# Kernel optimization log

Measured on AMD Instinct MI355X. Metric: run time of the kernel, lower is better.

The kernel has to match this reference:

```python
import jax, jax.numpy as jnp
import numpy as np

B, S, D, H, Dh, A_N = 2, 1024, 512, 8, 64, 18
HID = H * Dh        # 512, equals in_features
FFN = 4 * D         # SwiGLU hidden (ratio=4)
EPS = 1e-6


def rmsnorm(x, scale):
    return x * jax.lax.rsqrt(jnp.mean(jnp.square(x), axis=-1, keepdims=True) + EPS) * scale


def setup_inputs() -> dict:
    key = jax.random.key(0)
    ks = jax.random.split(key, 16)
    lecun = lambda k, shp: jax.random.normal(k, shp, jnp.float32) * (1.0 / np.sqrt(shp[0]))
    return {
        "x": jax.random.normal(ks[0], (B, S, D), jnp.float32),
        "action": jax.random.randint(ks[1], (B, S), 0, A_N, jnp.int32),
        "mask": jnp.zeros((B, S), jnp.int32),
        "carry": jnp.zeros((B, H, Dh, Dh), jnp.float32),
        "norm1_scale": jnp.ones((D,), jnp.float32),
        "wq": lecun(ks[2], (D, HID)),
        "wk": lecun(ks[3], (D, HID)),
        "wv": lecun(ks[4], (D, HID)),
        "w_beta": lecun(ks[5], (D, H)),
        "embed": jax.random.normal(ks[6], (A_N, HID), jnp.float32) * 0.02,
        "w_alpha": lecun(ks[7], (HID, H)),
        "w_bu": lecun(ks[8], (HID, HID)),
        "w_bv": lecun(ks[9], (HID, HID)),
        "norm_attn_scale": jnp.ones((HID,), jnp.float32),
        "w_out": lecun(ks[10], (HID, D)),
        "b_out": jnp.zeros((D,), jnp.float32),
        "norm2_scale": jnp.ones((D,), jnp.float32),
        "w_gate": lecun(ks[11], (D, FFN)),
        "w_val": lecun(ks[12], (D, FFN)),
        "w_ffn": lecun(ks[13], (FFN, D)),
    }


def reference(x, action, mask, carry, norm1_scale, wq, wk, wv, w_beta, embed,
              w_alpha, w_bu, w_bv, norm_attn_scale, w_out, b_out,
              norm2_scale, w_gate, w_val, w_ffn):
    dt = x.dtype
    h = rmsnorm(x, norm1_scale)
    # projections -> [B,S,H,Dh]
    q = jax.nn.silu(h @ wq).reshape(B, S, H, Dh)
    k = jax.nn.silu(h @ wk).reshape(B, S, H, Dh)
    v = (h @ wv).reshape(B, S, H, Dh)
    beta = jax.nn.sigmoid(h @ w_beta)                       # [B,S,H]
    ae = embed[action]                                      # [B,S,HID]
    alpha = jax.nn.sigmoid(ae @ w_alpha)                    # [B,S,H]
    b_u = (ae @ w_bu).reshape(B, S, H, Dh)
    b_v = (ae @ w_bv).reshape(B, S, H, Dh)
    q = q / (jnp.linalg.norm(q, axis=-1, keepdims=True) + EPS)
    k = k / (jnp.linalg.norm(k, axis=-1, keepdims=True) + EPS)
    eye = jnp.eye(Dh, dtype=dt)
    # delta = I - beta * k k^T   -> [B,S,H,Dh,Dh]
    delta = eye - beta[..., None, None] * jnp.einsum("bshi,bshj->bshij", k, k)
    m = mask.astype(dt)[:, :, None, None, None]
    decay = alpha[..., None, None] * delta * (1.0 - m)
    drift = jnp.einsum("bshi,bshj->bshij", b_u, b_v)
    write = beta[..., None, None] * jnp.einsum("bshi,bshj->bshij", v, k)
    update = drift @ delta + write

    def binop(lhs, rhs):
        a_i, b_i = lhs
        a_j, b_j = rhs
        return (a_i @ a_j, b_i @ a_j + b_j)

    cumdecay, hs = jax.lax.associative_scan(jax.vmap(binop), (decay, update), axis=1)
    hs = carry[:, None] @ cumdecay + hs                     # [B,S,H,Dh,Dh]
    attn = jnp.einsum("bshij,bshj->bshi", hs, q).reshape(B, S, HID)
    attn = rmsnorm(attn, norm_attn_scale)
    y = attn @ w_out + b_out
    skip = y + x
    h2 = rmsnorm(skip, norm2_scale)
    ffn = (jax.nn.silu(h2 @ w_gate) * (h2 @ w_val)) @ w_ffn
    return (hs[:, -1], skip + ffn)
```

## Files before the change

kernel.cpp:

```cpp
#include <hip/hip_runtime.h>
#include <hip/hip_bf16.h>
#include <cstdint>
#include <cstddef>

using bf16 = __hip_bfloat16;
typedef __attribute__((ext_vector_type(8))) short bf16x8;
typedef __attribute__((ext_vector_type(4))) float f32x4;

static constexpr int B_ = 2, S_ = 1024, D_ = 512, H_ = 8;
static constexpr int M_ = B_ * S_;
static constexpr int CHUNKS_ = 32, CLEN_ = 32;
static constexpr float EPS_ = 1e-6f;

__device__ __forceinline__ float sigmoidf_(float x) { return 1.0f / (1.0f + __expf(-x)); }

__device__ __forceinline__ short bf_hi(float v, float& rem) {
  bf16 h = __float2bfloat16(v);
  rem = v - __bfloat162float(h);
  return *(short*)&h;
}
__device__ __forceinline__ short bf_of(float v) {
  bf16 h = __float2bfloat16(v);
  return *(short*)&h;
}

struct TJob { const float* src; bf16* dst; int K, N, base, xf; };
struct TTab { TJob j[9]; };

__global__ __launch_bounds__(256) void k_transpose_all(TTab tab) {
  __shared__ float tile[32][33];
  int blk = blockIdx.x;
  int ji = 0;
#pragma unroll
  for (int t = 1; t < 9; ++t) if (tab.j[t].base <= blk) ji = t;
  const float* W = tab.j[ji].src;
  bf16* Wt = tab.j[ji].dst;
  int K = tab.j[ji].K, N = tab.j[ji].N, xf = tab.j[ji].xf;
  int rel = blk - tab.j[ji].base;
  int nb = N >> 5;
  int n0 = (rel % nb) * 32, k0 = (rel / nb) * 32;
  int tx = threadIdx.x, ty = threadIdx.y;
#pragma unroll
  for (int r = ty; r < 32; r += 8) tile[r][tx] = W[(size_t)(k0 + r) * N + n0 + tx];
  __syncthreads();
#pragma unroll
  for (int r = ty; r < 32; r += 8) {
    int n = n0 + r;
    int drow = n;
    if (xf == 1) drow = ((n >> 5) << 6) + (n & 31);
    else if (xf == 2) drow = ((n >> 5) << 6) + (n & 31) + 32;
    Wt[(size_t)drow * K + k0 + tx] = __float2bfloat16(tile[tx][r]);
  }
}

__global__ __launch_bounds__(256) void k_rmsnorm(const float* __restrict__ x,
                                                 const float* __restrict__ scale,
                                                 float* __restrict__ outf,
                                                 bf16* __restrict__ outb) {
  int m = blockIdx.x, tid = threadIdx.x;
  const float* row = x + (size_t)m * D_;
  float2 v = *(const float2*)(row + tid * 2);
  float ss = v.x * v.x + v.y * v.y;
#pragma unroll
  for (int o = 1; o < 64; o <<= 1) ss += __shfl_xor(ss, o);
  __shared__ float wsum[4];
  if ((tid & 63) == 0) wsum[tid >> 6] = ss;
  __syncthreads();
  float tot = wsum[0] + wsum[1] + wsum[2] + wsum[3];
  float rs = rsqrtf(tot * (1.0f / (float)D_) + EPS_);
  float2 sc = *(const float2*)(scale + tid * 2);
  float o0 = v.x * rs * sc.x, o1 = v.y * rs * sc.y;
  if (outf) {
    float2 o; o.x = o0; o.y = o1;
    *(float2*)(outf + (size_t)m * D_ + tid * 2) = o;
  }
  if (outb) {
    bf16* p = outb + (size_t)m * D_ + tid * 2;
    p[0] = __float2bfloat16(o0); p[1] = __float2bfloat16(o1);
  }
}

__global__ __launch_bounds__(256) void k_gather(const int* __restrict__ action,
                                                const float* __restrict__ embed,
                                                float* __restrict__ aef, bf16* __restrict__ aeb) {
  int m = blockIdx.x, tid = threadIdx.x;
  int a = action[m];
  float2 v = *(const float2*)(embed + (size_t)a * 512 + tid * 2);
  *(float2*)(aef + (size_t)m * 512 + tid * 2) = v;
  bf16* p = aeb + (size_t)m * 512 + tid * 2;
  p[0] = __float2bfloat16(v.x); p[1] = __float2bfloat16(v.y);
}

__global__ __launch_bounds__(256) void k_dot8x2(const float* __restrict__ hF,
                                                const float* __restrict__ aeF,
                                                const float* __restrict__ W1,
                                                const float* __restrict__ W2,
                                                float* __restrict__ o1,
                                                float* __restrict__ o2) {
  int m = blockIdx.x, tid = threadIdx.x;
  float x0 = hF[(size_t)m * D_ + tid], x1 = hF[(size_t)m * D_ + 256 + tid];
  float y0 = aeF[(size_t)m * D_ + tid], y1 = aeF[(size_t)m * D_ + 256 + tid];
  float p[8], q[8];
#pragma unroll
  for (int j = 0; j < 8; ++j) {
    p[j] = x0 * W1[tid * 8 + j] + x1 * W1[(tid + 256) * 8 + j];
    q[j] = y0 * W2[tid * 8 + j] + y1 * W2[(tid + 256) * 8 + j];
  }
#pragma unroll
  for (int j = 0; j < 8; ++j) {
#pragma unroll
    for (int o = 1; o < 64; o <<= 1) {
      p[j] += __shfl_xor(p[j], o);
      q[j] += __shfl_xor(q[j], o);
    }
  }
  __shared__ float sacc[4][16];
  if ((tid & 63) == 0) {
#pragma unroll
    for (int j = 0; j < 8; ++j) { sacc[tid >> 6][j] = p[j]; sacc[tid >> 6][8 + j] = q[j]; }
  }
  __syncthreads();
  if (tid < 8) {
    float s = sacc[0][tid] + sacc[1][tid] + sacc[2][tid] + sacc[3][tid];
    o1[(size_t)m * 8 + tid] = sigmoidf_(s);
  } else if (tid < 16) {
    int j = tid - 8;
    float s = sacc[0][8 + j] + sacc[1][8 + j] + sacc[2][8 + j] + sacc[3][8 + j];
    o2[(size_t)m * 8 + j] = sigmoidf_(s);
  }
}

__global__ __launch_bounds__(256) void k_qknorm_dots(float* __restrict__ qkv,
                                                     const float* __restrict__ buv,
                                                     const float* __restrict__ betaF,
                                                     const float* __restrict__ alphaF,
                                                     const int* __restrict__ mask,
                                                     float* __restrict__ scal8) {
  int blk = blockIdx.x * 4 + (threadIdx.x >> 6);
  int m = blk >> 3, h = blk & 7, t = threadIdx.x & 63;
  size_t qi = (size_t)m * 1536 + h * 64 + t;
  float q = qkv[qi], k = qkv[qi + 512];
  float bv = buv[(size_t)m * 1024 + 512 + h * 64 + t];
  float qs = q * q, ks = k * k;
#pragma unroll
  for (int o = 1; o < 64; o <<= 1) { qs += __shfl_xor(qs, o); ks += __shfl_xor(ks, o); }
  float qn = q / (sqrtf(qs) + EPS_);
  float kn = k / (sqrtf(ks) + EPS_);
  qkv[qi] = qn; qkv[qi + 512] = kn;
  float d0 = kn * qn, d1 = kn * bv, d2 = bv * qn;
#pragma unroll
  for (int o = 1; o < 64; o <<= 1) {
    d0 += __shfl_xor(d0, o); d1 += __shfl_xor(d1, o); d2 += __shfl_xor(d2, o);
  }
  if (t == 0) {
    int mh = m * 8 + h;
    float4 s4;
    s4.x = betaF[mh];
    s4.y = alphaF[mh] * (1.0f - (float)mask[m]);
    s4.z = d0; s4.w = d1;
    *(float4*)(scal8 + (size_t)mh * 8) = s4;
    scal8[(size_t)mh * 8 + 4] = d2;
  }
}

template <int EPI>
__global__ __launch_bounds__(256) void k_gemm2(const bf16* __restrict__ A,
                                               const bf16* __restrict__ Bt,
                                               void* __restrict__ Cv, int M, int N, int K,
                                               int actSplit, const float* __restrict__ bias,
                                               const float* __restrict__ res) {
  __shared__ bf16 As[2][64 * 32];
  __shared__ bf16 Bs[2][64 * 32];
  const int tid = threadIdx.x;
  const int wave = tid >> 6, lane = tid & 63;
  const int wm = wave >> 1, wn = wave & 1;
  const int m0 = blockIdx.y * 64, n0 = blockIdx.x * 64;
  const int lr = lane & 15, lg = lane >> 4;
  const int srow = (wave << 4) | (lane >> 2);
  const int skb = (lane & 3) << 3;
  const bf16* ga = A + (size_t)(m0 + srow) * K + skb;
  const bf16* gb = Bt + (size_t)(n0 + srow) * K + skb;

  f32x4 acc[2][2];
#pragma unroll
  for (int i = 0; i < 2; ++i)
#pragma unroll
    for (int j = 0; j < 2; ++j) acc[i][j] = (f32x4){0.f, 0.f, 0.f, 0.f};

  const int nk = K >> 5;
  int4 ar = *(const int4*)ga;
  int4 br = *(const int4*)gb;
  for (int t = 0; t < nk; ++t) {
    bf16* asb = &As[t & 1][0];
    bf16* bsb = &Bs[t & 1][0];
    *(int4*)(asb + tid * 8) = ar;
    *(int4*)(bsb + tid * 8) = br;
    __syncthreads();
    if (t + 1 < nk) {
      ar = *(const int4*)(ga + ((size_t)(t + 1) << 5));
      br = *(const int4*)(gb + ((size_t)(t + 1) << 5));
    }
    bf16x8 af[2], bfr[2];
#pragma unroll
    for (int mm = 0; mm < 2; ++mm)
      af[mm] = *(const bf16x8*)(asb + (wm * 32 + mm * 16 + lr) * 32 + lg * 8);
#pragma unroll
    for (int nn = 0; nn < 2; ++nn)
      bfr[nn] = *(const bf16x8*)(bsb + (wn * 32 + nn * 16 + lr) * 32 + lg * 8);
#pragma unroll
    for (int mm = 0; mm < 2; ++mm)
#pragma unroll
      for (int nn = 0; nn < 2; ++nn)
        acc[mm][nn] = __builtin_amdgcn_mfma_f32_16x16x32_bf16(af[mm], bfr[nn], acc[mm][nn], 0, 0, 0);
  }

  if constexpr (EPI == 4) {
    __syncthreads();
    float* gateL = (float*)&As[0][0];
    float* valL = (float*)&Bs[0][0];
    float* dstL = wn ? valL : gateL;
#pragma unroll
    for (int mm = 0; mm < 2; ++mm)
#pragma unroll
      for (int nn = 0; nn < 2; ++nn)
#pragma unroll
        for (int r = 0; r < 4; ++r)
          dstL[(wm * 32 + mm * 16 + lg * 4 + r) * 32 + nn * 16 + lr] = acc[mm][nn][r];
    __syncthreads();
    bf16* Cb = (bf16*)Cv;
    int row = tid >> 2, c0 = (tid & 3) * 8;
    bf16x8 o;
#pragma unroll
    for (int e = 0; e < 8; ++e) {
      float g = gateL[row * 32 + c0 + e];
      float v = valL[row * 32 + c0 + e];
      o[e] = bf_of(g * sigmoidf_(g) * v);
    }
    *(int4*)(Cb + (size_t)(m0 + row) * 2048 + blockIdx.x * 32 + c0) = *(int4*)&o;
  } else {
    float* C = (float*)Cv;
#pragma unroll
    for (int mm = 0; mm < 2; ++mm) {
#pragma unroll
      for (int nn = 0; nn < 2; ++nn) {
#pragma unroll
        for (int r = 0; r < 4; ++r) {
          int row = m0 + wm * 32 + mm * 16 + lg * 4 + r;
          int col = n0 + wn * 32 + nn * 16 + lr;
          float v = acc[mm][nn][r];
          if constexpr (EPI == 1) {
            if (col < actSplit) v = v * sigmoidf_(v);
          }
          if constexpr (EPI == 2) v += bias[col] + res[(size_t)row * N + col];
          if constexpr (EPI == 3) v += res[(size_t)row * N + col];
          C[(size_t)row * N + col] = v;
        }
      }
    }
  }
}

struct alignas(16) StepC {
  float k[16], bv[16], q[16];
  float v_i, bu_i, beta, g, kq, kbv, bvq;
};

__device__ __forceinline__ void load_stepc(StepC& sd,
    const float* __restrict__ qkv, const float* __restrict__ buv,
    const float* __restrict__ scal8, int m, int h, int i, int j0, bool withq) {
  const float* qb = qkv + (size_t)m * 1536 + h * 64;
  const float* bb = buv + (size_t)m * 1024 + h * 64;
#pragma unroll
  for (int p = 0; p < 4; ++p) *(float4*)&sd.k[p * 4] = *(const float4*)(qb + 512 + j0 + p * 4);
#pragma unroll
  for (int p = 0; p < 4; ++p) *(float4*)&sd.bv[p * 4] = *(const float4*)(bb + 512 + j0 + p * 4);
  if (withq) {
#pragma unroll
    for (int p = 0; p < 4; ++p) *(float4*)&sd.q[p * 4] = *(const float4*)(qb + j0 + p * 4);
  }
  sd.v_i = qb[1024 + i];
  sd.bu_i = bb[i];
  const float* sp = scal8 + (size_t)(m * 8 + h) * 8;
  float4 s4 = *(const float4*)sp;
  sd.beta = s4.x; sd.g = s4.y; sd.kq = s4.z; sd.kbv = s4.w;
  if (withq) sd.bvq = sp[4];
}

__device__ __forceinline__ void step_fold(float P[16], float U[16], const StepC& sd) {
  float Pk = 0.f, Uk = 0.f;
#pragma unroll
  for (int jj = 0; jj < 16; ++jj) { Pk += P[jj] * sd.k[jj]; Uk += U[jj] * sd.k[jj]; }
  Pk += __shfl_xor(Pk, 1); Pk += __shfl_xor(Pk, 2);
  Uk += __shfl_xor(Uk, 1); Uk += __shfl_xor(Uk, 2);
  float gb = sd.g * sd.beta;
  float cP = gb * Pk;
  float Ai = sd.beta * sd.v_i - gb * Uk - sd.bu_i * sd.beta * sd.kbv;
#pragma unroll
  for (int jj = 0; jj < 16; ++jj) {
    P[jj] = sd.g * P[jj] - cP * sd.k[jj];
    U[jj] = sd.g * U[jj] + Ai * sd.k[jj] + sd.bu_i * sd.bv[jj];
  }
}

__device__ __forceinline__ void step_apply(float hs[16], const StepC& sd,
                                           float* __restrict__ attn_addr, bool writer) {
  float u = 0.f, w = 0.f;
#pragma unroll
  for (int jj = 0; jj < 16; ++jj) { u += hs[jj] * sd.k[jj]; w += hs[jj] * sd.q[jj]; }
  u += __shfl_xor(u, 1); u += __shfl_xor(u, 2);
  w += __shfl_xor(w, 1); w += __shfl_xor(w, 2);
  float a_i = sd.beta * sd.v_i - sd.g * sd.beta * u;
  float c = sd.beta * sd.kbv;
#pragma unroll
  for (int jj = 0; jj < 16; ++jj) {
    float bvp = sd.bv[jj] - c * sd.k[jj];
    hs[jj] = sd.g * hs[jj] + a_i * sd.k[jj] + sd.bu_i * bvp;
  }
  if (writer) *attn_addr = sd.g * w + a_i * sd.kq + sd.bu_i * (sd.bvq - c * sd.kq);
}

__global__ __launch_bounds__(256) void k_scan_chunk(
    const float* __restrict__ qkv, const float* __restrict__ buv,
    const float* __restrict__ scal8, bf16* __restrict__ PtHi,
    bf16* __restrict__ PtLo, float* __restrict__ Ut) {
  int blk = blockIdx.x, bh = blk >> 5, c = blk & (CHUNKS_ - 1);
  int b = bh >> 3, h = bh & 7;
  int tid = threadIdx.x, i = tid >> 2, q4 = tid & 3, j0 = q4 * 16;
  alignas(16) float P[16], U[16];
#pragma unroll
  for (int jj = 0; jj < 16; ++jj) { P[jj] = (j0 + jj == i) ? 1.f : 0.f; U[jj] = 0.f; }
  int m0 = b * S_ + c * CLEN_;
  StepC A, Bs;
  load_stepc(A, qkv, buv, scal8, m0, h, i, j0, false);
  load_stepc(Bs, qkv, buv, scal8, m0 + 1, h, i, j0, false);
  for (int s = 0; s < CLEN_; s += 2) {
    step_fold(P, U, A);
    if (s + 2 < CLEN_) load_stepc(A, qkv, buv, scal8, m0 + s + 2, h, i, j0, false);
    step_fold(P, U, Bs);
    if (s + 3 < CLEN_) load_stepc(Bs, qkv, buv, scal8, m0 + s + 3, h, i, j0, false);
  }
  const size_t base = ((size_t)bh * CHUNKS_ + c) * 4096;
#pragma unroll
  for (int jj = 0; jj < 16; ++jj) {
    int j = j0 + jj;
    float pv = P[jj];
    float rem;
    short ph = bf_hi(pv, rem);
    short pl = bf_of(rem);
    ((short*)PtHi)[base + (size_t)j * 64 + i] = ph;
    ((short*)PtLo)[base + (size_t)j * 64 + i] = pl;
    Ut[base + (size_t)j * 64 + i] = U[jj];
  }
}

#define PREFETCH_(SET, CIDX)                                                     \
  {                                                                              \
    const size_t cbo_ = (size_t)(CIDX) * 4096;                                   \
    _Pragma("unroll") for (int mt = 0; mt < 4; ++mt) {                           \
      _Pragma("unroll") for (int ks = 0; ks < 2; ++ks) {                         \
        size_t off_ = cbo_ + (size_t)(16 * mt + lr) * 64 + ks * 32 + lg * 8;     \
        aH[SET][mt][ks] = *(const bf16x8*)(PH + off_);                           \
        aL[SET][mt][ks] = *(const bf16x8*)(PL + off_);                           \
      }                                                                          \
      _Pragma("unroll") for (int r = 0; r < 4; ++r)                              \
        u[SET][mt][r] = UB[cbo_ + (size_t)(16 * mt + 4 * lg + r) * 64 + col0 + lr]; \
    }                                                                            \
  }

#define CHAINSTEP_(SET, NSET, CIDX)                                              \
  {                                                                              \
    if ((CIDX) + 1 < CHUNKS_) PREFETCH_(NSET, (CIDX) + 1);                       \
    _Pragma("unroll") for (int mt = 0; mt < 4; ++mt)                             \
      _Pragma("unroll") for (int r = 0; r < 4; ++r)                              \
        HB[(size_t)(CIDX) * 4096 + (size_t)(16 * mt + 4 * lg + r) * 64 + col0 + lr] = st[mt][r]; \
    bf16x8 bH[2], bL[2];                                                         \
    _Pragma("unroll") for (int ks = 0; ks < 2; ++ks) {                           \
      _Pragma("unroll") for (int e = 0; e < 8; ++e) {                            \
        int src_ = (2 * (lg & 1) + (e >> 2)) * 16 + lr;                          \
        float va_ = __shfl(st[2 * ks][e & 3], src_);                             \
        float vb_ = __shfl(st[2 * ks + 1][e & 3], src_);                         \
        float bv_ = (lg & 2) ? vb_ : va_;                                        \
        float rem_;                                                              \
        bH[ks][e] = bf_hi(bv_, rem_);                                            \
        bL[ks][e] = bf_of(rem_);                                                 \
      }                                                                          \
    }                                                                            \
    f32x4 stn[4];                                                                \
    _Pragma("unroll") for (int mt = 0; mt < 4; ++mt) {                           \
      f32x4 a_ = u[SET][mt];                                                     \
      _Pragma("unroll") for (int ks = 0; ks < 2; ++ks) {                         \
        a_ = __builtin_amdgcn_mfma_f32_16x16x32_bf16(aH[SET][mt][ks], bH[ks], a_, 0, 0, 0); \
        a_ = __builtin_amdgcn_mfma_f32_16x16x32_bf16(aH[SET][mt][ks], bL[ks], a_, 0, 0, 0); \
        a_ = __builtin_amdgcn_mfma_f32_16x16x32_bf16(aL[SET][mt][ks], bH[ks], a_, 0, 0, 0); \
      }                                                                          \
      stn[mt] = a_;                                                              \
    }                                                                            \
    _Pragma("unroll") for (int mt = 0; mt < 4; ++mt) st[mt] = stn[mt];           \
  }

__global__ __launch_bounds__(64, 1) void k_chain3(
    const bf16* __restrict__ PtHi, const bf16* __restrict__ PtLo,
    const float* __restrict__ Ut, const float* __restrict__ carry,
    float* __restrict__ Hbuf, float* __restrict__ out_hs) {
  const int bh = blockIdx.x >> 2, cb = blockIdx.x & 3, col0 = cb * 16;
  const int lane = threadIdx.x & 63, lr = lane & 15, lg = lane >> 4;
  const short* PH = (const short*)PtHi + (size_t)bh * CHUNKS_ * 4096;
  const short* PL = (const short*)PtLo + (size_t)bh * CHUNKS_ * 4096;
  const float* UB = Ut + (size_t)bh * CHUNKS_ * 4096;
  float* HB = Hbuf + (size_t)bh * CHUNKS_ * 4096;

  f32x4 st[4];
#pragma unroll
  for (int mt = 0; mt < 4; ++mt)
    st[mt] = *(const f32x4*)(carry + ((size_t)bh * 64 + col0 + lr) * 64 + 16 * mt + 4 * lg);

  bf16x8 aH[2][4][2], aL[2][4][2];
  f32x4 u[2][4];
  PREFETCH_(0, 0);
  for (int c = 0; c < CHUNKS_; c += 2) {
    CHAINSTEP_(0, 1, c);
    CHAINSTEP_(1, 0, c + 1);
  }
#pragma unroll
  for (int mt = 0; mt < 4; ++mt)
    *(f32x4*)(out_hs + ((size_t)bh * 64 + col0 + lr) * 64 + 16 * mt + 4 * lg) = st[mt];
}

__global__ __launch_bounds__(256) void k_apply_chunk(
    const float* __restrict__ qkv, const float* __restrict__ buv,
    const float* __restrict__ scal8, const float* __restrict__ Hbuf,
    float* __restrict__ attn) {
  int blk = blockIdx.x, bh = blk >> 5, c = blk & (CHUNKS_ - 1);
  int b = bh >> 3, h = bh & 7;
  int tid = threadIdx.x, i = tid >> 2, q4 = tid & 3, j0 = q4 * 16;
  bool writer = (q4 == 0);
  alignas(16) float hs[16];
  const float* hb = Hbuf + ((size_t)bh * CHUNKS_ + c) * 4096;
#pragma unroll
  for (int jj = 0; jj < 16; ++jj) hs[jj] = hb[(size_t)(j0 + jj) * 64 + i];
  int m0 = b * S_ + c * CLEN_;
  StepC A, Bs;
  load_stepc(A, qkv, buv, scal8, m0, h, i, j0, true);
  load_stepc(Bs, qkv, buv, scal8, m0 + 1, h, i, j0, true);
  for (int s = 0; s < CLEN_; s += 2) {
    step_apply(hs, A, attn + ((size_t)(m0 + s) * 512 + h * 64 + i), writer);
    if (s + 2 < CLEN_) load_stepc(A, qkv, buv, scal8, m0 + s + 2, h, i, j0, true);
    step_apply(hs, Bs, attn + ((size_t)(m0 + s + 1) * 512 + h * 64 + i), writer);
    if (s + 3 < CLEN_) load_stepc(Bs, qkv, buv, scal8, m0 + s + 3, h, i, j0, true);
  }
}

extern "C" void kernel_launch(void* const* d_in, const int* in_sizes, int n_in,
                              void* d_out, int out_size, void* d_ws, size_t ws_size,
                              hipStream_t stream) {
  const float* x      = (const float*)d_in[0];
  const int*   action = (const int*)d_in[1];
  const int*   mask   = (const int*)d_in[2];
  const float* carry  = (const float*)d_in[3];
  const float* n1s    = (const float*)d_in[4];
  const float* wq     = (const float*)d_in[5];
  const float* wk     = (const float*)d_in[6];
  const float* wv     = (const float*)d_in[7];
  const float* wbeta  = (const float*)d_in[8];
  const float* embed  = (const float*)d_in[9];
  const float* walpha = (const float*)d_in[10];
  const float* wbu    = (const float*)d_in[11];
  const float* wbv    = (const float*)d_in[12];
  const float* nas    = (const float*)d_in[13];
  const float* wout   = (const float*)d_in[14];
  const float* bout   = (const float*)d_in[15];
  const float* n2s    = (const float*)d_in[16];
  const float* wgate  = (const float*)d_in[17];
  const float* wval   = (const float*)d_in[18];
  const float* wffn   = (const float*)d_in[19];

  float* out_hs  = (float*)d_out;
  float* out_ffn = (float*)d_out + 65536;

  char* p = (char*)d_ws;
  auto alloc = [&](size_t bytes) -> char* {
    char* r = p; p += (bytes + 255) & ~(size_t)255; return r;
  };
  bf16*  wqkvT = (bf16*)alloc((size_t)1536 * 512 * 2);
  bf16*  wbuvT = (bf16*)alloc((size_t)1024 * 512 * 2);
  bf16*  woutT = (bf16*)alloc((size_t)512 * 512 * 2);
  bf16*  wgvT  = (bf16*)alloc((size_t)4096 * 512 * 2);
  bf16*  wffnT = (bf16*)alloc((size_t)512 * 2048 * 2);
  float* hF    = (float*)alloc((size_t)M_ * 512 * 4);
  bf16*  hB    = (bf16*)alloc((size_t)M_ * 512 * 2);
  float* aeF   = (float*)alloc((size_t)M_ * 512 * 4);
  bf16*  aeB   = (bf16*)alloc((size_t)M_ * 512 * 2);
  float* qkvF  = (float*)alloc((size_t)M_ * 1536 * 4);
  float* buvF  = (float*)alloc((size_t)M_ * 1024 * 4);
  float* betaF = (float*)alloc((size_t)M_ * 8 * 4);
  float* alphaF= (float*)alloc((size_t)M_ * 8 * 4);
  float* scal8 = (float*)alloc((size_t)M_ * 8 * 8 * 4);
  float* attnF = (float*)alloc((size_t)M_ * 512 * 4);
  bf16*  attnB = (bf16*)alloc((size_t)M_ * 512 * 2);
  float* skipF = (float*)alloc((size_t)M_ * 512 * 4);
  bf16*  h2B   = (bf16*)alloc((size_t)M_ * 512 * 2);
  bf16*  ffnB  = (bf16*)alloc((size_t)M_ * 2048 * 2);
  char*  chunkWS = alloc((size_t)24 * 1024 * 1024);
  if ((size_t)(p - (char*)d_ws) > ws_size) return;

  constexpr size_t CELEMS = (size_t)16 * CHUNKS_ * 4096;
  bf16*  PtHi = (bf16*)(chunkWS);
  bf16*  PtLo = (bf16*)(chunkWS + CELEMS * 2);
  float* UtB  = (float*)(chunkWS + CELEMS * 4);
  float* Hbuf = (float*)(chunkWS + CELEMS * 8);

  TTab tab;
  tab.j[0] = {wq,    wqkvT,              512,  512,  0,    0};
  tab.j[1] = {wk,    wqkvT + 512 * 512,  512,  512,  256,  0};
  tab.j[2] = {wv,    wqkvT + 1024 * 512, 512,  512,  512,  0};
  tab.j[3] = {wbu,   wbuvT,              512,  512,  768,  0};
  tab.j[4] = {wbv,   wbuvT + 512 * 512,  512,  512,  1024, 0};
  tab.j[5] = {wout,  woutT,              512,  512,  1280, 0};
  tab.j[6] = {wgate, wgvT,               512,  2048, 1536, 1};
  tab.j[7] = {wval,  wgvT,               512,  2048, 2560, 2};
  tab.j[8] = {wffn,  wffnT,              2048, 512,  3584, 0};
  k_transpose_all<<<4608, dim3(32, 8), 0, stream>>>(tab);

  k_rmsnorm<<<M_, 256, 0, stream>>>(x, n1s, hF, hB);
  k_gather<<<M_, 256, 0, stream>>>(action, embed, aeF, aeB);

  k_gemm2<1><<<dim3(1536 / 64, M_ / 64), 256, 0, stream>>>(hB, wqkvT, qkvF, M_, 1536, 512, 1024, nullptr, nullptr);
  k_gemm2<0><<<dim3(1024 / 64, M_ / 64), 256, 0, stream>>>(aeB, wbuvT, buvF, M_, 1024, 512, 0, nullptr, nullptr);
  k_dot8x2<<<M_, 256, 0, stream>>>(hF, aeF, wbeta, walpha, betaF, alphaF);
  k_qknorm_dots<<<M_ * 2, 256, 0, stream>>>(qkvF, buvF, betaF, alphaF, mask, scal8);

  k_scan_chunk<<<16 * CHUNKS_, 256, 0, stream>>>(qkvF, buvF, scal8, PtHi, PtLo, UtB);
  k_chain3<<<64, 64, 0, stream>>>(PtHi, PtLo, UtB, carry, Hbuf, out_hs);
  k_apply_chunk<<<16 * CHUNKS_, 256, 0, stream>>>(qkvF, buvF, scal8, Hbuf, attnF);

  k_rmsnorm<<<M_, 256, 0, stream>>>(attnF, nas, nullptr, attnB);
  k_gemm2<2><<<dim3(512 / 64, M_ / 64), 256, 0, stream>>>(attnB, woutT, skipF, M_, 512, 512, 0, bout, x);
  k_rmsnorm<<<M_, 256, 0, stream>>>(skipF, n2s, nullptr, h2B);
  k_gemm2<4><<<dim3(4096 / 64, M_ / 64), 256, 0, stream>>>(h2B, wgvT, ffnB, M_, 4096, 512, 0, nullptr, nullptr);
  k_gemm2<3><<<dim3(512 / 64, M_ / 64), 256, 0, stream>>>(ffnB, wffnT, out_ffn, M_, 512, 2048, 0, nullptr, skipF);
}
```

Measured before the change: 227.6 us.

## Fold query projection into chunk scan and replace apply pass with MFMA GEMM

The chunk scan now also projects the running intra-chunk transition P and offset U onto each step's query, storing two per-step vectors. The per-chunk sequential apply pass is replaced by a small split-bf16 MFMA GEMM that multiplies each chunk's starting state by those projected queries and adds the offset term. This removes the second sequential 32-step recurrence over every chunk. The scan kernel does more per-step work and extra global writes. The workspace is also reorganized so the early activation buffers alias the chunk scratch region.

```diff
diff --git a/kernel.cpp b/kernel.cpp
--- a/kernel.cpp
+++ b/kernel.cpp
@@ -260,33 +260,33 @@
   }
 }
 
+
 struct alignas(16) StepC {
   float k[16], bv[16], q[16];
-  float v_i, bu_i, beta, g, kq, kbv, bvq;
+  float v_i, bu_i, beta, g, kbv;
 };
 
 __device__ __forceinline__ void load_stepc(StepC& sd,
     const float* __restrict__ qkv, const float* __restrict__ buv,
-    const float* __restrict__ scal8, int m, int h, int i, int j0, bool withq) {
+    const float* __restrict__ scal8, int m, int h, int i, int j0) {
   const float* qb = qkv + (size_t)m * 1536 + h * 64;
   const float* bb = buv + (size_t)m * 1024 + h * 64;
 #pragma unroll
   for (int p = 0; p < 4; ++p) *(float4*)&sd.k[p * 4] = *(const float4*)(qb + 512 + j0 + p * 4);
 #pragma unroll
   for (int p = 0; p < 4; ++p) *(float4*)&sd.bv[p * 4] = *(const float4*)(bb + 512 + j0 + p * 4);
-  if (withq) {
-#pragma unroll
-    for (int p = 0; p < 4; ++p) *(float4*)&sd.q[p * 4] = *(const float4*)(qb + j0 + p * 4);
-  }
+#pragma unroll
+  for (int p = 0; p < 4; ++p) *(float4*)&sd.q[p * 4] = *(const float4*)(qb + j0 + p * 4);
   sd.v_i = qb[1024 + i];
   sd.bu_i = bb[i];
   const float* sp = scal8 + (size_t)(m * 8 + h) * 8;
   float4 s4 = *(const float4*)sp;
-  sd.beta = s4.x; sd.g = s4.y; sd.kq = s4.z; sd.kbv = s4.w;
-  if (withq) sd.bvq = sp[4];
-}
-
-__device__ __forceinline__ void step_fold(float P[16], float U[16], const StepC& sd) {
+  sd.beta = s4.x; sd.g = s4.y; sd.kbv = s4.w;
+}
+
+__device__ __forceinline__ void step_fold_q(float P[16], float U[16], const StepC& sd,
+                                            float* __restrict__ qt_addr,
+                                            float* __restrict__ vt_addr, bool writer) {
   float Pk = 0.f, Uk = 0.f;
 #pragma unroll
   for (int jj = 0; jj < 16; ++jj) { Pk += P[jj] * sd.k[jj]; Uk += U[jj] * sd.k[jj]; }
@@ -295,49 +295,42 @@
   float gb = sd.g * sd.beta;
   float cP = gb * Pk;
   float Ai = sd.beta * sd.v_i - gb * Uk - sd.bu_i * sd.beta * sd.kbv;
+  float pq = 0.f, uq = 0.f;
 #pragma unroll
   for (int jj = 0; jj < 16; ++jj) {
     P[jj] = sd.g * P[jj] - cP * sd.k[jj];
     U[jj] = sd.g * U[jj] + Ai * sd.k[jj] + sd.bu_i * sd.bv[jj];
-  }
-}
-
-__device__ __forceinline__ void step_apply(float hs[16], const StepC& sd,
-                                           float* __restrict__ attn_addr, bool writer) {
-  float u = 0.f, w = 0.f;
-#pragma unroll
-  for (int jj = 0; jj < 16; ++jj) { u += hs[jj] * sd.k[jj]; w += hs[jj] * sd.q[jj]; }
-  u += __shfl_xor(u, 1); u += __shfl_xor(u, 2);
-  w += __shfl_xor(w, 1); w += __shfl_xor(w, 2);
-  float a_i = sd.beta * sd.v_i - sd.g * sd.beta * u;
-  float c = sd.beta * sd.kbv;
-#pragma unroll
-  for (int jj = 0; jj < 16; ++jj) {
-    float bvp = sd.bv[jj] - c * sd.k[jj];
-    hs[jj] = sd.g * hs[jj] + a_i * sd.k[jj] + sd.bu_i * bvp;
-  }
-  if (writer) *attn_addr = sd.g * w + a_i * sd.kq + sd.bu_i * (sd.bvq - c * sd.kq);
+    pq += P[jj] * sd.q[jj];
+    uq += U[jj] * sd.q[jj];
+  }
+  pq += __shfl_xor(pq, 1); pq += __shfl_xor(pq, 2);
+  uq += __shfl_xor(uq, 1); uq += __shfl_xor(uq, 2);
+  if (writer) { *qt_addr = pq; *vt_addr = uq; }
 }
 
 __global__ __launch_bounds__(256) void k_scan_chunk(
     const float* __restrict__ qkv, const float* __restrict__ buv,
     const float* __restrict__ scal8, bf16* __restrict__ PtHi,
-    bf16* __restrict__ PtLo, float* __restrict__ Ut) {
+    bf16* __restrict__ PtLo, float* __restrict__ Ut,
+    float* __restrict__ Qtb, float* __restrict__ Vtb) {
   int blk = blockIdx.x, bh = blk >> 5, c = blk & (CHUNKS_ - 1);
   int b = bh >> 3, h = bh & 7;
   int tid = threadIdx.x, i = tid >> 2, q4 = tid & 3, j0 = q4 * 16;
+  bool writer = (q4 == 0);
   alignas(16) float P[16], U[16];
 #pragma unroll
   for (int jj = 0; jj < 16; ++jj) { P[jj] = (j0 + jj == i) ? 1.f : 0.f; U[jj] = 0.f; }
   int m0 = b * S_ + c * CLEN_;
+  float* QT = Qtb + ((size_t)bh * CHUNKS_ + c) * (CLEN_ * 64);
+  float* VT = Vtb + ((size_t)bh * CHUNKS_ + c) * (CLEN_ * 64);
   StepC A, Bs;
-  load_stepc(A, qkv, buv, scal8, m0, h, i, j0, false);
-  load_stepc(Bs, qkv, buv, scal8, m0 + 1, h, i, j0, false);
+  load_stepc(A, qkv, buv, scal8, m0, h, i, j0);
+  load_stepc(Bs, qkv, buv, scal8, m0 + 1, h, i, j0);
   for (int s = 0; s < CLEN_; s += 2) {
-    step_fold(P, U, A);
-    if (s + 2 < CLEN_) load_stepc(A, qkv, buv, scal8, m0 + s + 2, h, i, j0, false);
-    step_fold(P, U, Bs);
-    if (s + 3 < CLEN_) load_stepc(Bs, qkv, buv, scal8, m0 + s + 3, h, i, j0, false);
+    step_fold_q(P, U, A, QT + s * 64 + i, VT + s * 64 + i, writer);
+    if (s + 2 < CLEN_) load_stepc(A, qkv, buv, scal8, m0 + s + 2, h, i, j0);
+    step_fold_q(P, U, Bs, QT + (s + 1) * 64 + i, VT + (s + 1) * 64 + i, writer);
+    if (s + 3 < CLEN_) load_stepc(Bs, qkv, buv, scal8, m0 + s + 3, h, i, j0);
   }
   const size_t base = ((size_t)bh * CHUNKS_ + c) * 4096;
 #pragma unroll
@@ -426,27 +419,57 @@
     *(f32x4*)(out_hs + ((size_t)bh * 64 + col0 + lr) * 64 + 16 * mt + 4 * lg) = st[mt];
 }
 
-__global__ __launch_bounds__(256) void k_apply_chunk(
-    const float* __restrict__ qkv, const float* __restrict__ buv,
-    const float* __restrict__ scal8, const float* __restrict__ Hbuf,
-    float* __restrict__ attn) {
-  int blk = blockIdx.x, bh = blk >> 5, c = blk & (CHUNKS_ - 1);
-  int b = bh >> 3, h = bh & 7;
-  int tid = threadIdx.x, i = tid >> 2, q4 = tid & 3, j0 = q4 * 16;
-  bool writer = (q4 == 0);
-  alignas(16) float hs[16];
-  const float* hb = Hbuf + ((size_t)bh * CHUNKS_ + c) * 4096;
-#pragma unroll
-  for (int jj = 0; jj < 16; ++jj) hs[jj] = hb[(size_t)(j0 + jj) * 64 + i];
-  int m0 = b * S_ + c * CLEN_;
-  StepC A, Bs;
-  load_stepc(A, qkv, buv, scal8, m0, h, i, j0, true);
-  load_stepc(Bs, qkv, buv, scal8, m0 + 1, h, i, j0, true);
-  for (int s = 0; s < CLEN_; s += 2) {
-    step_apply(hs, A, attn + ((size_t)(m0 + s) * 512 + h * 64 + i), writer);
-    if (s + 2 < CLEN_) load_stepc(A, qkv, buv, scal8, m0 + s + 2, h, i, j0, true);
-    step_apply(hs, Bs, attn + ((size_t)(m0 + s + 1) * 512 + h * 64 + i), writer);
-    if (s + 3 < CLEN_) load_stepc(Bs, qkv, buv, scal8, m0 + s + 3, h, i, j0, true);
+__global__ __launch_bounds__(256) void k_attn_gemm(
+    const float* __restrict__ Hbuf, const float* __restrict__ Qtb,
+    const float* __restrict__ Vtb, float* __restrict__ attn) {
+  const int blk = blockIdx.x, bh = blk >> 5, c = blk & (CHUNKS_ - 1);
+  const int b = bh >> 3, h = bh & 7;
+  const int tid = threadIdx.x, wave = tid >> 6, lane = tid & 63;
+  const int lr = lane & 15, lg = lane >> 4;
+  const float* H0 = Hbuf + ((size_t)bh * CHUNKS_ + c) * 4096;
+  const float* QT = Qtb + ((size_t)bh * CHUNKS_ + c) * (CLEN_ * 64);
+  const float* VT = Vtb + ((size_t)bh * CHUNKS_ + c) * (CLEN_ * 64);
+
+  bf16x8 aH[2], aL[2];
+#pragma unroll
+  for (int ks = 0; ks < 2; ++ks) {
+#pragma unroll
+    for (int e = 0; e < 8; ++e) {
+      float v = H0[(size_t)(ks * 32 + lg * 8 + e) * 64 + wave * 16 + lr];
+      float rem;
+      aH[ks][e] = bf_hi(v, rem);
+      aL[ks][e] = bf_of(rem);
+    }
+  }
+  f32x4 acc[2];
+#pragma unroll
+  for (int nt = 0; nt < 2; ++nt) {
+    f32x4 a = (f32x4){0.f, 0.f, 0.f, 0.f};
+#pragma unroll
+    for (int ks = 0; ks < 2; ++ks) {
+      const float* qp = QT + (size_t)(nt * 16 + lr) * 64 + ks * 32 + lg * 8;
+      bf16x8 bH, bL;
+#pragma unroll
+      for (int e = 0; e < 8; ++e) {
+        float rem;
+        bH[e] = bf_hi(qp[e], rem);
+        bL[e] = bf_of(rem);
+      }
+      a = __builtin_amdgcn_mfma_f32_16x16x32_bf16(aH[ks], bH, a, 0, 0, 0);
+      a = __builtin_amdgcn_mfma_f32_16x16x32_bf16(aH[ks], bL, a, 0, 0, 0);
+      a = __builtin_amdgcn_mfma_f32_16x16x32_bf16(aL[ks], bH, a, 0, 0, 0);
+    }
+    acc[nt] = a;
+  }
+  const int m0 = b * S_ + c * CLEN_;
+#pragma unroll
+  for (int nt = 0; nt < 2; ++nt) {
+    int s = nt * 16 + lr;
+    f32x4 vt = *(const f32x4*)(VT + (size_t)s * 64 + wave * 16 + lg * 4);
+    f32x4 o = acc[nt];
+#pragma unroll
+    for (int r = 0; r < 4; ++r) o[r] += vt[r];
+    *(f32x4*)(attn + (size_t)(m0 + s) * 512 + h * 64 + wave * 16 + lg * 4) = o;
   }
 }
 
@@ -486,10 +509,6 @@
   bf16*  woutT = (bf16*)alloc((size_t)512 * 512 * 2);
   bf16*  wgvT  = (bf16*)alloc((size_t)4096 * 512 * 2);
   bf16*  wffnT = (bf16*)alloc((size_t)512 * 2048 * 2);
-  float* hF    = (float*)alloc((size_t)M_ * 512 * 4);
-  bf16*  hB    = (bf16*)alloc((size_t)M_ * 512 * 2);
-  float* aeF   = (float*)alloc((size_t)M_ * 512 * 4);
-  bf16*  aeB   = (bf16*)alloc((size_t)M_ * 512 * 2);
   float* qkvF  = (float*)alloc((size_t)M_ * 1536 * 4);
   float* buvF  = (float*)alloc((size_t)M_ * 1024 * 4);
   float* betaF = (float*)alloc((size_t)M_ * 8 * 4);
@@ -500,14 +519,20 @@
   float* skipF = (float*)alloc((size_t)M_ * 512 * 4);
   bf16*  h2B   = (bf16*)alloc((size_t)M_ * 512 * 2);
   bf16*  ffnB  = (bf16*)alloc((size_t)M_ * 2048 * 2);
-  char*  chunkWS = alloc((size_t)24 * 1024 * 1024);
+  char*  tail  = alloc((size_t)32 * 1024 * 1024);
   if ((size_t)(p - (char*)d_ws) > ws_size) return;
 
-  constexpr size_t CELEMS = (size_t)16 * CHUNKS_ * 4096;
-  bf16*  PtHi = (bf16*)(chunkWS);
-  bf16*  PtLo = (bf16*)(chunkWS + CELEMS * 2);
-  float* UtB  = (float*)(chunkWS + CELEMS * 4);
-  float* Hbuf = (float*)(chunkWS + CELEMS * 8);
+  float* hF  = (float*)tail;
+  bf16*  hB  = (bf16*)(tail + ((size_t)4 << 20));
+  float* aeF = (float*)(tail + ((size_t)6 << 20));
+  bf16*  aeB = (bf16*)(tail + ((size_t)10 << 20));
+
+  bf16*  PtHi = (bf16*)tail;
+  bf16*  PtLo = (bf16*)(tail + ((size_t)4 << 20));
+  float* UtB  = (float*)(tail + ((size_t)8 << 20));
+  float* Hbuf = (float*)(tail + ((size_t)16 << 20));
+  float* Qtb  = (float*)(tail + ((size_t)24 << 20));
+  float* Vtb  = (float*)(tail + ((size_t)28 << 20));
 
   TTab tab;
   tab.j[0] = {wq,    wqkvT,              512,  512,  0,    0};
@@ -529,9 +554,9 @@
   k_dot8x2<<<M_, 256, 0, stream>>>(hF, aeF, wbeta, walpha, betaF, alphaF);
   k_qknorm_dots<<<M_ * 2, 256, 0, stream>>>(qkvF, buvF, betaF, alphaF, mask, scal8);
 
-  k_scan_chunk<<<16 * CHUNKS_, 256, 0, stream>>>(qkvF, buvF, scal8, PtHi, PtLo, UtB);
+  k_scan_chunk<<<16 * CHUNKS_, 256, 0, stream>>>(qkvF, buvF, scal8, PtHi, PtLo, UtB, Qtb, Vtb);
   k_chain3<<<64, 64, 0, stream>>>(PtHi, PtLo, UtB, carry, Hbuf, out_hs);
-  k_apply_chunk<<<16 * CHUNKS_, 256, 0, stream>>>(qkvF, buvF, scal8, Hbuf, attnF);
+  k_attn_gemm<<<16 * CHUNKS_, 256, 0, stream>>>(Hbuf, Qtb, Vtb, attnF);
 
   k_rmsnorm<<<M_, 256, 0, stream>>>(attnF, nas, nullptr, attnB);
   k_gemm2<2><<<dim3(512 / 64, M_ / 64), 256, 0, stream>>>(attnB, woutT, skipF, M_, 512, 512, 0, bout, x);
```

Measured after the change: 201.2 us. -11.6%, faster.
